# Performance work log

Measured on AMD Instinct MI355X. Metric: run time of the kernel, lower is better.

Reference implementation:

```python
import jax, jax.numpy as jnp
import numpy as np

B, TT, TS, H, O = 16, 512, 512, 1024, 1024


def setup_inputs() -> dict:
    key = jax.random.key(0)
    k1, k2, k3, k4, k5 = jax.random.split(key, 5)
    ht = jax.random.normal(k1, (B, TT, H), dtype=jnp.float32)
    hs = jax.random.normal(k2, (B, TS, H), dtype=jnp.float32)
    source = jax.random.randint(k3, (B, TS), 0, 10000, dtype=jnp.int32)
    # glorot-like scaling for weights
    W_a = jax.random.normal(k4, (H, H), dtype=jnp.float32) * (2.0 / (H + H)) ** 0.5
    W_c = jax.random.normal(k5, (2 * H, O), dtype=jnp.float32) * (2.0 / (2 * H + O)) ** 0.5
    b = jnp.zeros((O,), dtype=jnp.float32)
    return {"ht": ht, "hs": hs, "source": source, "W_a": W_a, "W_c": W_c, "b": b}


def reference(ht, hs, source, W_a, W_c, b):
    # score = ht . (hs @ W_a)^T : [B, Tt, Ts]
    keys = jnp.einsum('bsk,kl->bsl', hs, W_a)
    score = jnp.einsum('btk,bsk->bts', ht, keys)
    # stable exp with max subtraction (matches original manual softmax)
    score = jnp.exp(score - jnp.max(score, axis=-1, keepdims=True))
    # sequence mask from count of non-pad (non-zero) source tokens
    lens = jnp.sum((source != 0).astype(jnp.int32), axis=1)          # [B]
    mask = (jnp.arange(TS)[None, :] < lens[:, None]).astype(score.dtype)  # [B, Ts]
    score = score * mask[:, None, :]
    a = score / jnp.sum(score, axis=-1, keepdims=True)               # [B, Tt, Ts]
    c = jnp.einsum('bts,bsk->btk', a, hs)                            # context [B, Tt, H]
    h = jnp.concatenate([c, ht], axis=-1)                            # [B, Tt, 2H]
    return jnp.tanh(jnp.einsum('btk,kl->btl', h, W_c) + b)
```

## Files before the change

### kernel.cpp

```cpp
#include <hip/hip_runtime.h>
#include <math.h>

typedef unsigned short u16;
typedef unsigned int u32;

using f32x4 = __attribute__((ext_vector_type(4))) float;
using s16x8 = __attribute__((ext_vector_type(8))) short;
using f16x8 = __attribute__((ext_vector_type(8))) _Float16;
using u32x4 = __attribute__((ext_vector_type(4))) u32;

#define DEVI static __device__ __forceinline__

#define BB 16
#define TT 512
#define TS 512
#define HH 1024
#define OO 1024

DEVI void split_bf(float x, u16& hb, u16& lb) {
    u32 xb = __float_as_uint(x);
    float hf = __uint_as_float(xb & 0xffff0000u);
    hb = (u16)(xb >> 16);
    lb = (u16)(__float_as_uint(x - hf) >> 16);
}

DEVI float ub(u16 h) { return __uint_as_float((u32)h << 16); }

template <int PREC> struct FragT;
template <> struct FragT<0> { using T = s16x8; };
template <> struct FragT<1> { using T = f16x8; };

DEVI f32x4 mfma16(s16x8 a, s16x8 b, f32x4 c) {
    return __builtin_amdgcn_mfma_f32_16x16x32_bf16(a, b, c, 0, 0, 0);
}
DEVI f32x4 mfma16(f16x8 a, f16x8 b, f32x4 c) {
    return __builtin_amdgcn_mfma_f32_16x16x32_f16(a, b, c, 0, 0, 0);
}

DEVI void gl16(const void* g, void* l) {
    __builtin_amdgcn_global_load_lds(
        (__attribute__((address_space(1))) const void*)g,
        (__attribute__((address_space(3))) void*)l, 16, 0, 0);
}

__global__ void lens_kernel(const int* __restrict__ src, int* __restrict__ lens) {
    int b = blockIdx.x;
    int v = (src[b * TS + (int)threadIdx.x] != 0) ? 1 : 0;
    unsigned long long m = __ballot(v);
    __shared__ int part[8];
    if ((threadIdx.x & 63) == 0) part[threadIdx.x >> 6] = __popcll(m);
    __syncthreads();
    if (threadIdx.x == 0) {
        int s = 0;
#pragma unroll
        for (int i = 0; i < 8; ++i) s += part[i];
        lens[b] = s;
    }
}

template <int PREC>
__global__ void transpose_split_kernel(const float* __restrict__ src,
                                       u16* __restrict__ dhi, u16* __restrict__ dlo,
                                       int R, int C) {
    __shared__ float tile[32][33];
    long boff = (long)blockIdx.z * R * C;
    src += boff;
    dhi += boff;
    if (PREC == 0) dlo += boff;
    int c0 = blockIdx.x * 32, r0 = blockIdx.y * 32;
    int tx = threadIdx.x, ty = threadIdx.y;
#pragma unroll
    for (int i = 0; i < 32; i += 8)
        tile[ty + i][tx] = src[(long)(r0 + ty + i) * C + (c0 + tx)];
    __syncthreads();
#pragma unroll
    for (int i = 0; i < 32; i += 8) {
        float v = tile[tx][ty + i];
        long o = (long)(c0 + ty + i) * R + (r0 + tx);
        if constexpr (PREC == 0) {
            u16 hb, lb;
            split_bf(v, hb, lb);
            dhi[o] = hb;
            dlo[o] = lb;
        } else {
            dhi[o] = __builtin_bit_cast(u16, (_Float16)v);
        }
    }
}

__global__ void hs_prep_kernel(const float* __restrict__ src,
                               u16* __restrict__ rhi, u16* __restrict__ rlo,
                               u16* __restrict__ thi) {
    __shared__ float tile[32][33];
    long boff = (long)blockIdx.z * TS * HH;
    src += boff;
    rhi += boff;
    rlo += boff;
    thi += boff;
    int c0 = blockIdx.x * 32, r0 = blockIdx.y * 32;
    int tx = threadIdx.x, ty = threadIdx.y;
#pragma unroll
    for (int i = 0; i < 32; i += 8) {
        long o = (long)(r0 + ty + i) * HH + (c0 + tx);
        float v = src[o];
        tile[ty + i][tx] = v;
        u16 hb, lb;
        split_bf(v, hb, lb);
        rhi[o] = hb;
        rlo[o] = lb;
    }
    __syncthreads();
#pragma unroll
    for (int i = 0; i < 32; i += 8) {
        long o = (long)(c0 + ty + i) * TS + (r0 + tx);
        thi[o] = __builtin_bit_cast(u16, (_Float16)tile[tx][ty + i]);
    }
}

__global__ void softmax_mask_kernel(u16* __restrict__ h0, u16* __restrict__ l0,
                                    const u16* __restrict__ h1, const u16* __restrict__ l1,
                                    const int* __restrict__ lens) {
    long row = blockIdx.x;
    int len = lens[blockIdx.x >> 9];
    int lane = threadIdx.x;
    long o = row * TS + 8 * lane;
    s16x8 vh0 = *(const s16x8*)(h0 + o);
    s16x8 vl0 = *(const s16x8*)(l0 + o);
    s16x8 vh1 = *(const s16x8*)(h1 + o);
    s16x8 vl1 = *(const s16x8*)(l1 + o);
    float f[8];
#pragma unroll
    for (int i = 0; i < 8; ++i)
        f[i] = (ub((u16)vh0[i]) + ub((u16)vl0[i])) + (ub((u16)vh1[i]) + ub((u16)vl1[i]));
    float m = f[0];
#pragma unroll
    for (int i = 1; i < 8; ++i) m = fmaxf(m, f[i]);
#pragma unroll
    for (int os = 32; os > 0; os >>= 1) m = fmaxf(m, __shfl_xor(m, os));
    float e[8];
    float sum = 0.f;
#pragma unroll
    for (int i = 0; i < 8; ++i) {
        e[i] = (8 * lane + i < len) ? expf(f[i] - m) : 0.f;
        sum += e[i];
    }
#pragma unroll
    for (int os = 32; os > 0; os >>= 1) sum += __shfl_xor(sum, os);
    float inv = 1.0f / sum;
    f16x8 p;
#pragma unroll
    for (int i = 0; i < 8; ++i) p[i] = (_Float16)(e[i] * inv);
    *(f16x8*)(h0 + o) = p;
}

template <int PREC, int ASRC, int EPI, int TERMS, int KSPLIT, bool SWZ>
__global__ __launch_bounds__(256, 2)
void gemm_u(const u16* __restrict__ Ahi, const u16* __restrict__ Alo,
            const float* __restrict__ Af,
            const u16* __restrict__ Bhi, const u16* __restrict__ Blo,
            float* __restrict__ C, u16* __restrict__ Chi, u16* __restrict__ Clo,
            const float* __restrict__ bias,
            int M, int N, int K, int lda, int ldb,
            long sA, long sB, long sC, long sKh) {
    int bx, by, bz;
    if (SWZ) {
        int id = blockIdx.x;
        int ns = ((id & 7) << 6) | (id >> 3);
        bx = ns & 7;
        by = ns >> 3;
        bz = 0;
    } else {
        bx = blockIdx.x;
        by = blockIdx.y;
        bz = blockIdx.z;
    }
    int kh = 0;
    if (KSPLIT == 2) {
        kh = bz & 1;
        bz >>= 1;
    }
    if (ASRC == 0) {
        Ahi += (long)bz * sA + (long)kh * K;
        if (TERMS == 3) Alo += (long)bz * sA + (long)kh * K;
    } else if (ASRC == 1) {
        Af += (long)bz * sA + (long)kh * K;
    }
    Bhi += (long)bz * sB + (long)kh * K;
    if (TERMS == 3) Blo += (long)bz * sB + (long)kh * K;

    int n0 = bx * 128;
    int m0 = by * 128;

    constexpr int NARR = (TERMS == 3) ? 4 : 2;
    constexpr int AH = 0, AL = 1;
    constexpr int BH = (TERMS == 3) ? 2 : 1;
    constexpr int BL = 3;
    __shared__ u16 lds[2][NARR * 4096];

    int tid = threadIdx.x;
    int lane = tid & 63;
    int wave = tid >> 6;
    int wm = (wave >> 1) * 64;
    int wn = (wave & 1) * 64;
    int fr = lane & 15;
    int kq = lane >> 4;

    f32x4 acc[4][4];
#pragma unroll
    for (int i = 0; i < 4; ++i)
#pragma unroll
        for (int j = 0; j < 4; ++j) acc[i][j] = (f32x4){0.f, 0.f, 0.f, 0.f};

    auto stage_gl = [&](int bufi, int arr, const u16* g, int r0, int ldg, int k0) {
#pragma unroll
        for (int h = 0; h < 2; ++h) {
            int vt = tid + h * 256;
            int row = vt >> 2;
            int ls = (vt & 3) ^ ((row >> 1) & 3);
            const u16* gp = g + (long)(r0 + row) * ldg + (k0 + 8 * ls);
            u16* lp = &lds[bufi][arr * 4096 + (vt >> 6) * 512];
            gl16(gp, lp);
        }
    };

    auto stage_a_f32 = [&](int bufi, const float* g, int ldg, int kk) {
        int r = tid >> 1;
        int hf = (tid & 1) * 16;
        const float* p = g + (long)(m0 + r) * ldg + kk + hf;
        float4 a0 = *(const float4*)(p + 0);
        float4 a1 = *(const float4*)(p + 4);
        float4 a2 = *(const float4*)(p + 8);
        float4 a3 = *(const float4*)(p + 12);
        float fv[16] = {a0.x, a0.y, a0.z, a0.w, a1.x, a1.y, a1.z, a1.w,
                        a2.x, a2.y, a2.z, a2.w, a3.x, a3.y, a3.z, a3.w};
        u16 hb[16], lb[16];
#pragma unroll
        for (int i = 0; i < 16; ++i) {
            if constexpr (PREC == 0)
                split_bf(fv[i], hb[i], lb[i]);
            else
                hb[i] = __builtin_bit_cast(u16, (_Float16)fv[i]);
        }
        int sw = (r >> 1) & 3;
        int ls0 = hf >> 3;
        u32x4 h0 = {(u32)hb[0] | ((u32)hb[1] << 16), (u32)hb[2] | ((u32)hb[3] << 16),
                    (u32)hb[4] | ((u32)hb[5] << 16), (u32)hb[6] | ((u32)hb[7] << 16)};
        u32x4 h1 = {(u32)hb[8] | ((u32)hb[9] << 16), (u32)hb[10] | ((u32)hb[11] << 16),
                    (u32)hb[12] | ((u32)hb[13] << 16), (u32)hb[14] | ((u32)hb[15] << 16)};
        u16* ah = &lds[bufi][AH * 4096 + r * 32];
        *(u32x4*)(ah + (((ls0 + 0) ^ sw) << 3)) = h0;
        *(u32x4*)(ah + (((ls0 + 1) ^ sw) << 3)) = h1;
        if constexpr (TERMS == 3) {
            u32x4 l0 = {(u32)lb[0] | ((u32)lb[1] << 16), (u32)lb[2] | ((u32)lb[3] << 16),
                        (u32)lb[4] | ((u32)lb[5] << 16), (u32)lb[6] | ((u32)lb[7] << 16)};
            u32x4 l1 = {(u32)lb[8] | ((u32)lb[9] << 16), (u32)lb[10] | ((u32)lb[11] << 16),
                        (u32)lb[12] | ((u32)lb[13] << 16), (u32)lb[14] | ((u32)lb[15] << 16)};
            u16* al = &lds[bufi][AL * 4096 + r * 32];
            *(u32x4*)(al + (((ls0 + 0) ^ sw) << 3)) = l0;
            *(u32x4*)(al + (((ls0 + 1) ^ sw) << 3)) = l1;
        }
    };

    auto stage = [&](int bufi, int t) {
        int k0 = t * 32;
        stage_gl(bufi, BH, Bhi, n0, ldb, k0);
        if (TERMS == 3) stage_gl(bufi, BL, Blo, n0, ldb, k0);
        if (ASRC == 0) {
            stage_gl(bufi, AH, Ahi, m0, lda, k0);
            if (TERMS == 3) stage_gl(bufi, AL, Alo, m0, lda, k0);
        } else if (ASRC == 1) {
            stage_a_f32(bufi, Af, lda, k0);
        } else {
            if (k0 < HH)
                stage_gl(bufi, AH, Ahi, m0, lda, k0);
            else
                stage_a_f32(bufi, Af, lda, k0 - HH);
        }
    };

    const int NT = K / 32;
    stage(0, 0);
    __syncthreads();
    int cur = 0;
    using FT = typename FragT<PREC>::T;
    for (int t = 0; t < NT; ++t) {
        if (t + 1 < NT) stage(cur ^ 1, t + 1);

        const u16* L = lds[cur];
        FT afh[4], afl[4], bfh[4], bfl[4];
#pragma unroll
        for (int i = 0; i < 4; ++i) {
            int ra = wm + i * 16 + fr;
            int rb = wn + i * 16 + fr;
            int oa = ra * 32 + ((kq ^ ((ra >> 1) & 3)) << 3);
            int ob = rb * 32 + ((kq ^ ((rb >> 1) & 3)) << 3);
            afh[i] = *(const FT*)(L + AH * 4096 + oa);
            bfh[i] = *(const FT*)(L + BH * 4096 + ob);
            if (TERMS == 3) {
                afl[i] = *(const FT*)(L + AL * 4096 + oa);
                bfl[i] = *(const FT*)(L + BL * 4096 + ob);
            }
        }
#pragma unroll
        for (int i = 0; i < 4; ++i)
#pragma unroll
            for (int j = 0; j < 4; ++j) {
                acc[i][j] = mfma16(afh[i], bfh[j], acc[i][j]);
                if (TERMS == 3) {
                    acc[i][j] = mfma16(afl[i], bfh[j], acc[i][j]);
                    acc[i][j] = mfma16(afh[i], bfl[j], acc[i][j]);
                }
            }
        __syncthreads();
        cur ^= 1;
    }

    long obase = (long)bz * sC + (long)kh * sKh;
    int fq = (lane >> 4) * 4;
#pragma unroll
    for (int i = 0; i < 4; ++i)
#pragma unroll
        for (int j = 0; j < 4; ++j)
#pragma unroll
            for (int g = 0; g < 4; ++g) {
                int row = m0 + wm + i * 16 + fq + g;
                int col = n0 + wn + j * 16 + fr;
                long idx = obase + (long)row * N + col;
                float v = acc[i][j][g];
                if constexpr (EPI == 1) {
                    u16 h2, l2;
                    split_bf(v, h2, l2);
                    Chi[idx] = h2;
                    Clo[idx] = l2;
                } else if constexpr (EPI == 2) {
                    float x = v + bias[col];
                    float t2 = __expf(2.f * x);
                    C[idx] = 1.f - 2.f * __builtin_amdgcn_rcpf(t2 + 1.f);
                } else {
                    Chi[idx] = __builtin_bit_cast(u16, (_Float16)v);
                }
            }
}

extern "C" void kernel_launch(void* const* d_in, const int* in_sizes, int n_in,
                              void* d_out, int out_size, void* d_ws, size_t ws_size,
                              hipStream_t stream) {
    const float* ht = (const float*)d_in[0];
    const float* hs = (const float*)d_in[1];
    const int* source = (const int*)d_in[2];
    const float* Wa = (const float*)d_in[3];
    const float* Wc = (const float*)d_in[4];
    const float* bias = (const float*)d_in[5];
    float* out = (float*)d_out;

    char* w = (char*)d_ws;
    size_t off = 0;
    auto alloc = [&](size_t bytes) -> void* {
        void* p = w + off;
        off += (bytes + 255) & ~(size_t)255;
        return p;
    };
    int* lens = (int*)alloc(256);
    u16* keysHi = (u16*)alloc((size_t)BB * TS * HH * 2);
    u16* keysLo = (u16*)alloc((size_t)BB * TS * HH * 2);
    u16* hsRHi = (u16*)alloc((size_t)BB * TS * HH * 2);
    u16* hsRLo = (u16*)alloc((size_t)BB * TS * HH * 2);
    u16* hsTHi = (u16*)alloc((size_t)BB * HH * TS * 2);
    u16* WaTHi = (u16*)alloc((size_t)HH * HH * 2);
    u16* WaTLo = (u16*)alloc((size_t)HH * HH * 2);
    u16* scoreH0 = hsRHi;
    u16* scoreH1 = hsRHi + (size_t)BB * TT * TS;
    u16* scoreL0 = hsRLo;
    u16* scoreL1 = hsRLo + (size_t)BB * TT * TS;
    u16* cHi = keysHi;
    u16* WcTHi = scoreL0;
    u16* prob = scoreH0;

    lens_kernel<<<BB, TS, 0, stream>>>(source, lens);
    transpose_split_kernel<0><<<dim3(HH / 32, HH / 32, 1), dim3(32, 8), 0, stream>>>(
        Wa, WaTHi, WaTLo, HH, HH);
    hs_prep_kernel<<<dim3(HH / 32, TS / 32, BB), dim3(32, 8), 0, stream>>>(
        hs, hsRHi, hsRLo, hsTHi);

    gemm_u<0, 0, 1, 3, 1, true><<<dim3(512), 256, 0, stream>>>(
        hsRHi, hsRLo, nullptr, WaTHi, WaTLo,
        nullptr, keysHi, keysLo, nullptr,
        BB * TS, HH, HH, HH, HH, 0, 0, 0, 0);

    gemm_u<0, 1, 1, 3, 2, false><<<dim3(TS / 128, TT / 128, 2 * BB), 256, 0, stream>>>(
        nullptr, nullptr, ht, keysHi, keysLo,
        nullptr, scoreH0, scoreL0, nullptr,
        TT, TS, HH / 2, HH, HH,
        (long)TT * HH, (long)TS * HH, (long)TT * TS, (long)BB * TT * TS);

    softmax_mask_kernel<<<BB * TT, 64, 0, stream>>>(scoreH0, scoreL0, scoreH1, scoreL1, lens);

    gemm_u<1, 0, 3, 1, 1, false><<<dim3(HH / 128, TT / 128, BB), 256, 0, stream>>>(
        prob, nullptr, nullptr, hsTHi, nullptr,
        nullptr, cHi, nullptr, nullptr,
        TT, HH, TS, TS, TS,
        (long)TT * TS, (long)HH * TS, (long)TT * HH, 0);

    transpose_split_kernel<1><<<dim3(OO / 32, 2 * HH / 32, 1), dim3(32, 8), 0, stream>>>(
        Wc, WcTHi, nullptr, 2 * HH, OO);

    gemm_u<1, 2, 2, 1, 1, true><<<dim3(512), 256, 0, stream>>>(
        cHi, nullptr, ht, WcTHi, nullptr,
        out, nullptr, nullptr, bias,
        BB * TT, OO, 2 * HH, HH, 2 * HH, 0, 0, 0, 0);
}
```

Baseline: 195.9 us.

## Rework GEMMs into 256x128 tiles with triple-buffered async LDS pipeline

New measurement: 212.7 us. 8.6% more time.

```diff
diff --git a/kernel.cpp b/kernel.cpp
--- a/kernel.cpp
+++ b/kernel.cpp
@@ -7,7 +7,7 @@
 using f32x4 = __attribute__((ext_vector_type(4))) float;
 using s16x8 = __attribute__((ext_vector_type(8))) short;
 using f16x8 = __attribute__((ext_vector_type(8))) _Float16;
-using u32x4 = __attribute__((ext_vector_type(4))) u32;
+using u16x4 = __attribute__((ext_vector_type(4))) u16;
 
 #define DEVI static __device__ __forceinline__
 
@@ -115,6 +115,34 @@
         long o = (long)(c0 + ty + i) * TS + (r0 + tx);
         thi[o] = __builtin_bit_cast(u16, (_Float16)tile[tx][ty + i]);
     }
+}
+
+__global__ void ht_prep_kernel(const float* __restrict__ ht,
+                               u16* __restrict__ bhi, u16* __restrict__ blo) {
+    long i = ((long)blockIdx.x * 256 + threadIdx.x) * 4;
+    float4 v = *(const float4*)(ht + i);
+    float f[4] = {v.x, v.y, v.z, v.w};
+    u16x4 h, l;
+#pragma unroll
+    for (int j = 0; j < 4; ++j) {
+        u16 hb, lb;
+        split_bf(f[j], hb, lb);
+        h[j] = hb;
+        l[j] = lb;
+    }
+    *(u16x4*)(bhi + i) = h;
+    *(u16x4*)(blo + i) = l;
+}
+
+__global__ void htf_prep_kernel(const float* __restrict__ ht, u16* __restrict__ f) {
+    long i = ((long)blockIdx.x * 256 + threadIdx.x) * 8;
+    float4 v0 = *(const float4*)(ht + i);
+    float4 v1 = *(const float4*)(ht + i + 4);
+    float fv[8] = {v0.x, v0.y, v0.z, v0.w, v1.x, v1.y, v1.z, v1.w};
+    f16x8 o;
+#pragma unroll
+    for (int j = 0; j < 8; ++j) o[j] = (_Float16)fv[j];
+    *(f16x8*)(f + i) = o;
 }
 
 __global__ void softmax_mask_kernel(u16* __restrict__ h0, u16* __restrict__ l0,
@@ -153,22 +181,32 @@
     *(f16x8*)(h0 + o) = p;
 }
 
-template <int PREC, int ASRC, int EPI, int TERMS, int KSPLIT, bool SWZ>
-__global__ __launch_bounds__(256, 2)
-void gemm_u(const u16* __restrict__ Ahi, const u16* __restrict__ Alo,
-            const float* __restrict__ Af,
+template <int PREC, int TERMS, int EPI, int ACON, int KSPLIT, int SWZ>
+__global__ __launch_bounds__(512, 2)
+void gemm_p(const u16* __restrict__ Ahi, const u16* __restrict__ Alo,
+            const u16* __restrict__ A2,
             const u16* __restrict__ Bhi, const u16* __restrict__ Blo,
             float* __restrict__ C, u16* __restrict__ Chi, u16* __restrict__ Clo,
             const float* __restrict__ bias,
-            int M, int N, int K, int lda, int ldb,
+            int N, int K, int lda, int ldb,
             long sA, long sB, long sC, long sKh) {
-    int bx, by, bz;
+    constexpr int SUBS = (TERMS == 3) ? 1 : 2;
+    constexpr int BKI = 32 * SUBS;
+    constexpr int SUBU = (TERMS == 3) ? 24576 : 12288;
+    constexpr int BUFU = 24576;
+    constexpr int AHo = 0;
+    constexpr int ALof = 8192;
+    constexpr int BHo = (TERMS == 3) ? 16384 : 8192;
+    constexpr int BLof = 20480;
+
+    __shared__ u16 lds[3 * BUFU];
+
+    int bx, by, bz = 0;
     if (SWZ) {
         int id = blockIdx.x;
-        int ns = ((id & 7) << 6) | (id >> 3);
+        int ns = ((id & 7) << 5) | (id >> 3);
+        by = ns >> 3;
         bx = ns & 7;
-        by = ns >> 3;
-        bz = 0;
     } else {
         bx = blockIdx.x;
         by = blockIdx.y;
@@ -179,23 +217,12 @@
         kh = bz & 1;
         bz >>= 1;
     }
-    if (ASRC == 0) {
+    if (!ACON) {
         Ahi += (long)bz * sA + (long)kh * K;
         if (TERMS == 3) Alo += (long)bz * sA + (long)kh * K;
-    } else if (ASRC == 1) {
-        Af += (long)bz * sA + (long)kh * K;
     }
     Bhi += (long)bz * sB + (long)kh * K;
     if (TERMS == 3) Blo += (long)bz * sB + (long)kh * K;
-
-    int n0 = bx * 128;
-    int m0 = by * 128;
-
-    constexpr int NARR = (TERMS == 3) ? 4 : 2;
-    constexpr int AH = 0, AL = 1;
-    constexpr int BH = (TERMS == 3) ? 2 : 1;
-    constexpr int BL = 3;
-    __shared__ u16 lds[2][NARR * 4096];
 
     int tid = threadIdx.x;
     int lane = tid & 63;
@@ -204,6 +231,8 @@
     int wn = (wave & 1) * 64;
     int fr = lane & 15;
     int kq = lane >> 4;
+    int m0 = by * 256;
+    int n0 = bx * 128;
 
     f32x4 acc[4][4];
 #pragma unroll
@@ -211,108 +240,90 @@
 #pragma unroll
         for (int j = 0; j < 4; ++j) acc[i][j] = (f32x4){0.f, 0.f, 0.f, 0.f};
 
-    auto stage_gl = [&](int bufi, int arr, const u16* g, int r0, int ldg, int k0) {
-#pragma unroll
-        for (int h = 0; h < 2; ++h) {
-            int vt = tid + h * 256;
+    auto stage_arr = [&](int dst, const u16* g, int r0, int ldg, int k0, int cnt) {
+#pragma unroll
+        for (int h = 0; h < cnt; ++h) {
+            int vt = tid + h * 512;
             int row = vt >> 2;
             int ls = (vt & 3) ^ ((row >> 1) & 3);
             const u16* gp = g + (long)(r0 + row) * ldg + (k0 + 8 * ls);
-            u16* lp = &lds[bufi][arr * 4096 + (vt >> 6) * 512];
+            u16* lp = lds + dst + ((tid & ~63) + h * 512) * 8;
             gl16(gp, lp);
         }
     };
-
-    auto stage_a_f32 = [&](int bufi, const float* g, int ldg, int kk) {
-        int r = tid >> 1;
-        int hf = (tid & 1) * 16;
-        const float* p = g + (long)(m0 + r) * ldg + kk + hf;
-        float4 a0 = *(const float4*)(p + 0);
-        float4 a1 = *(const float4*)(p + 4);
-        float4 a2 = *(const float4*)(p + 8);
-        float4 a3 = *(const float4*)(p + 12);
-        float fv[16] = {a0.x, a0.y, a0.z, a0.w, a1.x, a1.y, a1.z, a1.w,
-                        a2.x, a2.y, a2.z, a2.w, a3.x, a3.y, a3.z, a3.w};
-        u16 hb[16], lb[16];
-#pragma unroll
-        for (int i = 0; i < 16; ++i) {
-            if constexpr (PREC == 0)
-                split_bf(fv[i], hb[i], lb[i]);
-            else
-                hb[i] = __builtin_bit_cast(u16, (_Float16)fv[i]);
-        }
-        int sw = (r >> 1) & 3;
-        int ls0 = hf >> 3;
-        u32x4 h0 = {(u32)hb[0] | ((u32)hb[1] << 16), (u32)hb[2] | ((u32)hb[3] << 16),
-                    (u32)hb[4] | ((u32)hb[5] << 16), (u32)hb[6] | ((u32)hb[7] << 16)};
-        u32x4 h1 = {(u32)hb[8] | ((u32)hb[9] << 16), (u32)hb[10] | ((u32)hb[11] << 16),
-                    (u32)hb[12] | ((u32)hb[13] << 16), (u32)hb[14] | ((u32)hb[15] << 16)};
-        u16* ah = &lds[bufi][AH * 4096 + r * 32];
-        *(u32x4*)(ah + (((ls0 + 0) ^ sw) << 3)) = h0;
-        *(u32x4*)(ah + (((ls0 + 1) ^ sw) << 3)) = h1;
-        if constexpr (TERMS == 3) {
-            u32x4 l0 = {(u32)lb[0] | ((u32)lb[1] << 16), (u32)lb[2] | ((u32)lb[3] << 16),
-                        (u32)lb[4] | ((u32)lb[5] << 16), (u32)lb[6] | ((u32)lb[7] << 16)};
-            u32x4 l1 = {(u32)lb[8] | ((u32)lb[9] << 16), (u32)lb[10] | ((u32)lb[11] << 16),
-                        (u32)lb[12] | ((u32)lb[13] << 16), (u32)lb[14] | ((u32)lb[15] << 16)};
-            u16* al = &lds[bufi][AL * 4096 + r * 32];
-            *(u32x4*)(al + (((ls0 + 0) ^ sw) << 3)) = l0;
-            *(u32x4*)(al + (((ls0 + 1) ^ sw) << 3)) = l1;
+    auto stage = [&](int bi, int t) {
+#pragma unroll
+        for (int s = 0; s < SUBS; ++s) {
+            int ks = t * BKI + s * 32;
+            int sb = bi * BUFU + s * ((TERMS == 3) ? 0 : SUBU);
+            if (ACON) {
+                if (ks < HH)
+                    stage_arr(sb + AHo, Ahi, m0, lda, ks, 2);
+                else
+                    stage_arr(sb + AHo, A2, m0, lda, ks - HH, 2);
+            } else {
+                stage_arr(sb + AHo, Ahi, m0, lda, ks, 2);
+                if (TERMS == 3) stage_arr(sb + ALof, Alo, m0, lda, ks, 2);
+            }
+            stage_arr(sb + BHo, Bhi, n0, ldb, ks, 1);
+            if (TERMS == 3) stage_arr(sb + BLof, Blo, n0, ldb, ks, 1);
         }
     };
 
-    auto stage = [&](int bufi, int t) {
-        int k0 = t * 32;
-        stage_gl(bufi, BH, Bhi, n0, ldb, k0);
-        if (TERMS == 3) stage_gl(bufi, BL, Blo, n0, ldb, k0);
-        if (ASRC == 0) {
-            stage_gl(bufi, AH, Ahi, m0, lda, k0);
-            if (TERMS == 3) stage_gl(bufi, AL, Alo, m0, lda, k0);
-        } else if (ASRC == 1) {
-            stage_a_f32(bufi, Af, lda, k0);
-        } else {
-            if (k0 < HH)
-                stage_gl(bufi, AH, Ahi, m0, lda, k0);
-            else
-                stage_a_f32(bufi, Af, lda, k0 - HH);
-        }
-    };
-
-    const int NT = K / 32;
+    const int NTI = K / BKI;
     stage(0, 0);
-    __syncthreads();
-    int cur = 0;
+    stage(1, 1);
+    stage(2, 2);
+    asm volatile("s_waitcnt vmcnt(12)" ::: "memory");
+    __builtin_amdgcn_sched_barrier(0);
+    __builtin_amdgcn_s_barrier();
+    __builtin_amdgcn_sched_barrier(0);
+
     using FT = typename FragT<PREC>::T;
-    for (int t = 0; t < NT; ++t) {
-        if (t + 1 < NT) stage(cur ^ 1, t + 1);
-
-        const u16* L = lds[cur];
-        FT afh[4], afl[4], bfh[4], bfl[4];
-#pragma unroll
-        for (int i = 0; i < 4; ++i) {
-            int ra = wm + i * 16 + fr;
-            int rb = wn + i * 16 + fr;
-            int oa = ra * 32 + ((kq ^ ((ra >> 1) & 3)) << 3);
-            int ob = rb * 32 + ((kq ^ ((rb >> 1) & 3)) << 3);
-            afh[i] = *(const FT*)(L + AH * 4096 + oa);
-            bfh[i] = *(const FT*)(L + BH * 4096 + ob);
-            if (TERMS == 3) {
-                afl[i] = *(const FT*)(L + AL * 4096 + oa);
-                bfl[i] = *(const FT*)(L + BL * 4096 + ob);
-            }
-        }
-#pragma unroll
-        for (int i = 0; i < 4; ++i)
-#pragma unroll
-            for (int j = 0; j < 4; ++j) {
-                acc[i][j] = mfma16(afh[i], bfh[j], acc[i][j]);
+    for (int t = 0; t < NTI; ++t) {
+        if (t >= 1 && t + 2 < NTI) stage((t + 2) % 3, t + 2);
+
+        const u16* Lb = lds + (t % 3) * BUFU;
+#pragma unroll
+        for (int s = 0; s < SUBS; ++s) {
+            const u16* Ls = Lb + s * SUBU;
+            FT afh[4], afl[4], bfh[4], bfl[4];
+#pragma unroll
+            for (int i = 0; i < 4; ++i) {
+                int ra = wm + i * 16 + fr;
+                int rb = wn + i * 16 + fr;
+                int oa = ra * 32 + ((kq ^ ((ra >> 1) & 3)) << 3);
+                int ob = rb * 32 + ((kq ^ ((rb >> 1) & 3)) << 3);
+                afh[i] = *(const FT*)(Ls + AHo + oa);
+                bfh[i] = *(const FT*)(Ls + BHo + ob);
                 if (TERMS == 3) {
-                    acc[i][j] = mfma16(afl[i], bfh[j], acc[i][j]);
-                    acc[i][j] = mfma16(afh[i], bfl[j], acc[i][j]);
+                    afl[i] = *(const FT*)(Ls + ALof + oa);
+                    bfl[i] = *(const FT*)(Ls + BLof + ob);
                 }
             }
-        __syncthreads();
-        cur ^= 1;
+            __builtin_amdgcn_s_setprio(1);
+#pragma unroll
+            for (int i = 0; i < 4; ++i)
+#pragma unroll
+                for (int j = 0; j < 4; ++j) {
+                    acc[i][j] = mfma16(afh[i], bfh[j], acc[i][j]);
+                    if (TERMS == 3) {
+                        acc[i][j] = mfma16(afl[i], bfh[j], acc[i][j]);
+                        acc[i][j] = mfma16(afh[i], bfl[j], acc[i][j]);
+                    }
+                }
+            __builtin_amdgcn_s_setprio(0);
+        }
+        if (t < NTI - 1) {
+            __builtin_amdgcn_sched_barrier(0);
+            if (t + 2 < NTI)
+                asm volatile("s_waitcnt vmcnt(6)" ::: "memory");
+            else
+                asm volatile("s_waitcnt vmcnt(0)" ::: "memory");
+            __builtin_amdgcn_sched_barrier(0);
+            __builtin_amdgcn_s_barrier();
+            __builtin_amdgcn_sched_barrier(0);
+        }
     }
 
     long obase = (long)bz * sC + (long)kh * sKh;
@@ -374,38 +385,43 @@
     u16* scoreL1 = hsRLo + (size_t)BB * TT * TS;
     u16* cHi = keysHi;
     u16* WcTHi = scoreL0;
+    u16* htF = hsTHi;
     u16* prob = scoreH0;
+    u16* htBHi = (u16*)d_out;
+    u16* htBLo = (u16*)d_out + (size_t)BB * TT * HH;
 
     lens_kernel<<<BB, TS, 0, stream>>>(source, lens);
     transpose_split_kernel<0><<<dim3(HH / 32, HH / 32, 1), dim3(32, 8), 0, stream>>>(
         Wa, WaTHi, WaTLo, HH, HH);
     hs_prep_kernel<<<dim3(HH / 32, TS / 32, BB), dim3(32, 8), 0, stream>>>(
         hs, hsRHi, hsRLo, hsTHi);
-
-    gemm_u<0, 0, 1, 3, 1, true><<<dim3(512), 256, 0, stream>>>(
+    ht_prep_kernel<<<(BB * TT * HH) / (256 * 4), 256, 0, stream>>>(ht, htBHi, htBLo);
+
+    gemm_p<0, 3, 1, 0, 1, 1><<<256, 512, 0, stream>>>(
         hsRHi, hsRLo, nullptr, WaTHi, WaTLo,
         nullptr, keysHi, keysLo, nullptr,
-        BB * TS, HH, HH, HH, HH, 0, 0, 0, 0);
-
-    gemm_u<0, 1, 1, 3, 2, false><<<dim3(TS / 128, TT / 128, 2 * BB), 256, 0, stream>>>(
-        nullptr, nullptr, ht, keysHi, keysLo,
+        HH, HH, HH, HH, 0, 0, 0, 0);
+
+    gemm_p<0, 3, 1, 0, 2, 0><<<dim3(4, 2, 32), 512, 0, stream>>>(
+        htBHi, htBLo, nullptr, keysHi, keysLo,
         nullptr, scoreH0, scoreL0, nullptr,
-        TT, TS, HH / 2, HH, HH,
+        TS, HH / 2, HH, HH,
         (long)TT * HH, (long)TS * HH, (long)TT * TS, (long)BB * TT * TS);
 
     softmax_mask_kernel<<<BB * TT, 64, 0, stream>>>(scoreH0, scoreL0, scoreH1, scoreL1, lens);
 
-    gemm_u<1, 0, 3, 1, 1, false><<<dim3(HH / 128, TT / 128, BB), 256, 0, stream>>>(
+    gemm_p<1, 1, 3, 0, 1, 0><<<dim3(8, 2, BB), 512, 0, stream>>>(
         prob, nullptr, nullptr, hsTHi, nullptr,
         nullptr, cHi, nullptr, nullptr,
-        TT, HH, TS, TS, TS,
+        HH, TS, TS, TS,
         (long)TT * TS, (long)HH * TS, (long)TT * HH, 0);
 
+    htf_prep_kernel<<<(BB * TT * HH) / (256 * 8), 256, 0, stream>>>(ht, htF);
     transpose_split_kernel<1><<<dim3(OO / 32, 2 * HH / 32, 1), dim3(32, 8), 0, stream>>>(
         Wc, WcTHi, nullptr, 2 * HH, OO);
 
-    gemm_u<1, 2, 2, 1, 1, true><<<dim3(512), 256, 0, stream>>>(
-        cHi, nullptr, ht, WcTHi, nullptr,
+    gemm_p<1, 1, 2, 1, 1, 1><<<256, 512, 0, stream>>>(
+        cHi, nullptr, htF, WcTHi, nullptr,
         out, nullptr, nullptr, bias,
-        BB * TT, OO, 2 * HH, HH, 2 * HH, 0, 0, 0, 0);
-}
+        OO, 2 * HH, HH, 2 * HH, 0, 0, 0, 0);
+}
```

## Add 256x128 triple-buffered async GEMM and pre-convert ht to fp16

Applied to the files above, without the earlier changes.

Measured after the change: 197.4 us. No clear change (+0.8%).

```diff
diff --git a/kernel.cpp b/kernel.cpp
--- a/kernel.cpp
+++ b/kernel.cpp
@@ -115,6 +115,17 @@
         long o = (long)(c0 + ty + i) * TS + (r0 + tx);
         thi[o] = __builtin_bit_cast(u16, (_Float16)tile[tx][ty + i]);
     }
+}
+
+__global__ void htf_prep_kernel(const float* __restrict__ ht, u16* __restrict__ f) {
+    long i = ((long)blockIdx.x * 256 + threadIdx.x) * 8;
+    float4 v0 = *(const float4*)(ht + i);
+    float4 v1 = *(const float4*)(ht + i + 4);
+    float fv[8] = {v0.x, v0.y, v0.z, v0.w, v1.x, v1.y, v1.z, v1.w};
+    f16x8 o;
+#pragma unroll
+    for (int j = 0; j < 8; ++j) o[j] = (_Float16)fv[j];
+    *(f16x8*)(f + i) = o;
 }
 
 __global__ void softmax_mask_kernel(u16* __restrict__ h0, u16* __restrict__ l0,
@@ -151,6 +162,178 @@
 #pragma unroll
     for (int i = 0; i < 8; ++i) p[i] = (_Float16)(e[i] * inv);
     *(f16x8*)(h0 + o) = p;
+}
+
+template <int PREC, int TERMS, int EPI, int ACON, int KSPLIT, int SWZ>
+__global__ __launch_bounds__(512, 2)
+void gemm_p(const u16* __restrict__ Ahi, const u16* __restrict__ Alo,
+            const u16* __restrict__ A2,
+            const u16* __restrict__ Bhi, const u16* __restrict__ Blo,
+            float* __restrict__ C, u16* __restrict__ Chi, u16* __restrict__ Clo,
+            const float* __restrict__ bias,
+            int N, int K, int lda, int ldb,
+            long sA, long sB, long sC, long sKh) {
+    constexpr int SUBS = (TERMS == 3) ? 1 : 2;
+    constexpr int BKI = 32 * SUBS;
+    constexpr int SUBU = (TERMS == 3) ? 24576 : 12288;
+    constexpr int BUFU = 24576;
+    constexpr int AHo = 0;
+    constexpr int ALof = 8192;
+    constexpr int BHo = (TERMS == 3) ? 16384 : 8192;
+    constexpr int BLof = 20480;
+
+    __shared__ u16 lds[3 * BUFU];
+
+    int bx, by, bz = 0;
+    if (SWZ) {
+        int id = blockIdx.x;
+        int ns = ((id & 7) << 5) | (id >> 3);
+        by = ns >> 3;
+        bx = ns & 7;
+    } else {
+        bx = blockIdx.x;
+        by = blockIdx.y;
+        bz = blockIdx.z;
+    }
+    int kh = 0;
+    if (KSPLIT == 2) {
+        kh = bz & 1;
+        bz >>= 1;
+    }
+    if (!ACON) {
+        Ahi += (long)bz * sA + (long)kh * K;
+        if (TERMS == 3) Alo += (long)bz * sA + (long)kh * K;
+    }
+    Bhi += (long)bz * sB + (long)kh * K;
+    if (TERMS == 3) Blo += (long)bz * sB + (long)kh * K;
+
+    int tid = threadIdx.x;
+    int lane = tid & 63;
+    int wave = tid >> 6;
+    int wm = (wave >> 1) * 64;
+    int wn = (wave & 1) * 64;
+    int fr = lane & 15;
+    int kq = lane >> 4;
+    int m0 = by * 256;
+    int n0 = bx * 128;
+
+    f32x4 acc[4][4];
+#pragma unroll
+    for (int i = 0; i < 4; ++i)
+#pragma unroll
+        for (int j = 0; j < 4; ++j) acc[i][j] = (f32x4){0.f, 0.f, 0.f, 0.f};
+
+    auto stage_arr = [&](int dst, const u16* g, int r0, int ldg, int k0, int cnt) {
+#pragma unroll
+        for (int h = 0; h < cnt; ++h) {
+            int vt = tid + h * 512;
+            int row = vt >> 2;
+            int ls = (vt & 3) ^ ((row >> 1) & 3);
+            const u16* gp = g + (long)(r0 + row) * ldg + (k0 + 8 * ls);
+            u16* lp = lds + dst + ((tid & ~63) + h * 512) * 8;
+            gl16(gp, lp);
+        }
+    };
+    auto stage = [&](int bi, int t) {
+#pragma unroll
+        for (int s = 0; s < SUBS; ++s) {
+            int ks = t * BKI + s * 32;
+            int sb = bi * BUFU + s * ((TERMS == 3) ? 0 : SUBU);
+            if (ACON) {
+                if (ks < HH)
+                    stage_arr(sb + AHo, Ahi, m0, lda, ks, 2);
+                else
+                    stage_arr(sb + AHo, A2, m0, lda, ks - HH, 2);
+            } else {
+                stage_arr(sb + AHo, Ahi, m0, lda, ks, 2);
+                if (TERMS == 3) stage_arr(sb + ALof, Alo, m0, lda, ks, 2);
+            }
+            stage_arr(sb + BHo, Bhi, n0, ldb, ks, 1);
+            if (TERMS == 3) stage_arr(sb + BLof, Blo, n0, ldb, ks, 1);
+        }
+    };
+
+    const int NTI = K / BKI;
+    stage(0, 0);
+    stage(1, 1);
+    stage(2, 2);
+    asm volatile("s_waitcnt vmcnt(12)" ::: "memory");
+    __builtin_amdgcn_sched_barrier(0);
+    __builtin_amdgcn_s_barrier();
+    __builtin_amdgcn_sched_barrier(0);
+
+    using FT = typename FragT<PREC>::T;
+    for (int t = 0; t < NTI; ++t) {
+        if (t >= 1 && t + 2 < NTI) stage((t + 2) % 3, t + 2);
+
+        const u16* Lb = lds + (t % 3) * BUFU;
+#pragma unroll
+        for (int s = 0; s < SUBS; ++s) {
+            const u16* Ls = Lb + s * SUBU;
+            FT afh[4], afl[4], bfh[4], bfl[4];
+#pragma unroll
+            for (int i = 0; i < 4; ++i) {
+                int ra = wm + i * 16 + fr;
+                int rb = wn + i * 16 + fr;
+                int oa = ra * 32 + ((kq ^ ((ra >> 1) & 3)) << 3);
+                int ob = rb * 32 + ((kq ^ ((rb >> 1) & 3)) << 3);
+                afh[i] = *(const FT*)(Ls + AHo + oa);
+                bfh[i] = *(const FT*)(Ls + BHo + ob);
+                if (TERMS == 3) {
+                    afl[i] = *(const FT*)(Ls + ALof + oa);
+                    bfl[i] = *(const FT*)(Ls + BLof + ob);
+                }
+            }
+            __builtin_amdgcn_s_setprio(1);
+#pragma unroll
+            for (int i = 0; i < 4; ++i)
+#pragma unroll
+                for (int j = 0; j < 4; ++j) {
+                    acc[i][j] = mfma16(afh[i], bfh[j], acc[i][j]);
+                    if (TERMS == 3) {
+                        acc[i][j] = mfma16(afl[i], bfh[j], acc[i][j]);
+                        acc[i][j] = mfma16(afh[i], bfl[j], acc[i][j]);
+                    }
+                }
+            __builtin_amdgcn_s_setprio(0);
+        }
+        if (t < NTI - 1) {
+            __builtin_amdgcn_sched_barrier(0);
+            if (t + 2 < NTI)
+                asm volatile("s_waitcnt vmcnt(6)" ::: "memory");
+            else
+                asm volatile("s_waitcnt vmcnt(0)" ::: "memory");
+            __builtin_amdgcn_sched_barrier(0);
+            __builtin_amdgcn_s_barrier();
+            __builtin_amdgcn_sched_barrier(0);
+        }
+    }
+
+    long obase = (long)bz * sC + (long)kh * sKh;
+    int fq = (lane >> 4) * 4;
+#pragma unroll
+    for (int i = 0; i < 4; ++i)
+#pragma unroll
+        for (int j = 0; j < 4; ++j)
+#pragma unroll
+            for (int g = 0; g < 4; ++g) {
+                int row = m0 + wm + i * 16 + fq + g;
+                int col = n0 + wn + j * 16 + fr;
+                long idx = obase + (long)row * N + col;
+                float v = acc[i][j][g];
+                if constexpr (EPI == 1) {
+                    u16 h2, l2;
+                    split_bf(v, h2, l2);
+                    Chi[idx] = h2;
+                    Clo[idx] = l2;
+                } else if constexpr (EPI == 2) {
+                    float x = v + bias[col];
+                    float t2 = __expf(2.f * x);
+                    C[idx] = 1.f - 2.f * __builtin_amdgcn_rcpf(t2 + 1.f);
+                } else {
+                    Chi[idx] = __builtin_bit_cast(u16, (_Float16)v);
+                }
+            }
 }
 
 template <int PREC, int ASRC, int EPI, int TERMS, int KSPLIT, bool SWZ>
@@ -268,13 +451,8 @@
         if (ASRC == 0) {
             stage_gl(bufi, AH, Ahi, m0, lda, k0);
             if (TERMS == 3) stage_gl(bufi, AL, Alo, m0, lda, k0);
-        } else if (ASRC == 1) {
+        } else {
             stage_a_f32(bufi, Af, lda, k0);
-        } else {
-            if (k0 < HH)
-                stage_gl(bufi, AH, Ahi, m0, lda, k0);
-            else
-                stage_a_f32(bufi, Af, lda, k0 - HH);
         }
     };
 
@@ -374,6 +552,7 @@
     u16* scoreL1 = hsRLo + (size_t)BB * TT * TS;
     u16* cHi = keysHi;
     u16* WcTHi = scoreL0;
+    u16* htF = hsTHi;
     u16* prob = scoreH0;
 
     lens_kernel<<<BB, TS, 0, stream>>>(source, lens);
@@ -382,10 +561,10 @@
     hs_prep_kernel<<<dim3(HH / 32, TS / 32, BB), dim3(32, 8), 0, stream>>>(
         hs, hsRHi, hsRLo, hsTHi);
 
-    gemm_u<0, 0, 1, 3, 1, true><<<dim3(512), 256, 0, stream>>>(
+    gemm_p<0, 3, 1, 0, 1, 1><<<256, 512, 0, stream>>>(
         hsRHi, hsRLo, nullptr, WaTHi, WaTLo,
         nullptr, keysHi, keysLo, nullptr,
-        BB * TS, HH, HH, HH, HH, 0, 0, 0, 0);
+        HH, HH, HH, HH, 0, 0, 0, 0);
 
     gemm_u<0, 1, 1, 3, 2, false><<<dim3(TS / 128, TT / 128, 2 * BB), 256, 0, stream>>>(
         nullptr, nullptr, ht, keysHi, keysLo,
@@ -395,17 +574,18 @@
 
     softmax_mask_kernel<<<BB * TT, 64, 0, stream>>>(scoreH0, scoreL0, scoreH1, scoreL1, lens);
 
-    gemm_u<1, 0, 3, 1, 1, false><<<dim3(HH / 128, TT / 128, BB), 256, 0, stream>>>(
+    gemm_p<1, 1, 3, 0, 1, 0><<<dim3(8, 2, BB), 512, 0, stream>>>(
         prob, nullptr, nullptr, hsTHi, nullptr,
         nullptr, cHi, nullptr, nullptr,
-        TT, HH, TS, TS, TS,
+        HH, TS, TS, TS,
         (long)TT * TS, (long)HH * TS, (long)TT * HH, 0);
 
+    htf_prep_kernel<<<(BB * TT * HH) / (256 * 8), 256, 0, stream>>>(ht, htF);
     transpose_split_kernel<1><<<dim3(OO / 32, 2 * HH / 32, 1), dim3(32, 8), 0, stream>>>(
         Wc, WcTHi, nullptr, 2 * HH, OO);
 
-    gemm_u<1, 2, 2, 1, 1, true><<<dim3(512), 256, 0, stream>>>(
-        cHi, nullptr, ht, WcTHi, nullptr,
+    gemm_p<1, 1, 2, 1, 1, 1><<<256, 512, 0, stream>>>(
+        cHi, nullptr, htF, WcTHi, nullptr,
         out, nullptr, nullptr, bias,
-        BB * TT, OO, 2 * HH, HH, 2 * HH, 0, 0, 0, 0);
-}
+        OO, 2 * HH, HH, 2 * HH, 0, 0, 0, 0);
+}
```
